# Optimization experiments

Hardware: AMD Instinct MI355X
Metric: run time of the kernel (lower is better)

The kernel has to match this reference:

```python
import jax, jax.numpy as jnp
import numpy as np

NUM_SEGMENTS = 2048
EPS = 1e-6

def setup_inputs() -> dict:
    key = jax.random.key(0)
    k1, k2 = jax.random.split(key)
    N, D = 1000000, 64
    x = jax.random.normal(k1, (N, D), dtype=jnp.float32)
    seg = jnp.sort(jax.random.randint(k2, (N,), 0, NUM_SEGMENTS, dtype=jnp.int32))
    return {"x": x, "seg": seg}

def reference(x, seg):
    # Per-segment SCALAR min/max over all nodes and features of each graph,
    # matching torch's x.min()/x.max() on each unbatched segment.
    row_min = jnp.min(x, axis=1)  # [N]
    row_max = jnp.max(x, axis=1)  # [N]
    g_min = jax.ops.segment_min(row_min, seg, num_segments=NUM_SEGMENTS)  # [G]
    g_max = jax.ops.segment_max(row_max, seg, num_segments=NUM_SEGMENTS)  # [G]
    mn = g_min[seg][:, None]  # [N,1]
    mx = g_max[seg][:, None]  # [N,1]
    return (x - mn) / (mx - mn + EPS)
```

## Files before the change

### kernel.cpp

```cpp
#include <hip/hip_runtime.h>

#define NSEG 2048
#define EPS 1e-6f

__device__ __forceinline__ unsigned enc(float f) {
    unsigned u = __float_as_uint(f);
    return (u & 0x80000000u) ? ~u : (u | 0x80000000u);
}
__device__ __forceinline__ float dec(unsigned k) {
    unsigned u = (k & 0x80000000u) ? (k & 0x7FFFFFFFu) : ~k;
    return __uint_as_float(u);
}

__global__ void init_k(unsigned* __restrict__ mn_k, unsigned* __restrict__ mx_k) {
    int i = blockIdx.x * blockDim.x + threadIdx.x;
    if (i < NSEG) {
        mn_k[i] = 0xFFFFFFFFu;
        mx_k[i] = 0u;
    }
}

__global__ __launch_bounds__(256) void pass1(const float4* __restrict__ x4,
                                             const int* __restrict__ seg,
                                             unsigned* __restrict__ mn_k,
                                             unsigned* __restrict__ mx_k,
                                             int nrows) {
    int row = blockIdx.x * 256 + threadIdx.x;
    if (row >= nrows) return;
    const float4* xr = x4 + (long)row * 16;
    float lmin = INFINITY, lmax = -INFINITY;
#pragma unroll
    for (int j = 0; j < 16; ++j) {
        float4 v = xr[j];
        lmin = fminf(lmin, fminf(fminf(v.x, v.y), fminf(v.z, v.w)));
        lmax = fmaxf(lmax, fmaxf(fmaxf(v.x, v.y), fmaxf(v.z, v.w)));
    }
    int s = seg[row];
    int first = __shfl(s, 0);
    if (__all(s == first)) {
#pragma unroll
        for (int off = 32; off; off >>= 1) {
            lmin = fminf(lmin, __shfl_xor(lmin, off));
            lmax = fmaxf(lmax, __shfl_xor(lmax, off));
        }
        if ((threadIdx.x & 63) == 0) {
            atomicMin(&mn_k[first], enc(lmin));
            atomicMax(&mx_k[first], enc(lmax));
        }
    } else {
        atomicMin(&mn_k[s], enc(lmin));
        atomicMax(&mx_k[s], enc(lmax));
    }
}

__global__ void scalek(const unsigned* __restrict__ mn_k,
                       const unsigned* __restrict__ mx_k,
                       float2* __restrict__ prm) {
    int i = blockIdx.x * blockDim.x + threadIdx.x;
    if (i < NSEG) {
        float mn = dec(mn_k[i]);
        float mx = dec(mx_k[i]);
        float2 p;
        p.x = mn;
        p.y = 1.0f / (mx - mn + EPS);
        prm[i] = p;
    }
}

__global__ __launch_bounds__(256) void pass2(const float4* __restrict__ x4,
                                             const int* __restrict__ seg,
                                             const float2* __restrict__ prm,
                                             float4* __restrict__ out4,
                                             long n4) {
    long g = (long)blockIdx.x * 256 + threadIdx.x;
    if (g >= n4) return;
    int row = (int)(g >> 4);
    int s = seg[row];
    float2 p = prm[s];
    float4 v = x4[g];
    float4 o;
    o.x = (v.x - p.x) * p.y;
    o.y = (v.y - p.x) * p.y;
    o.z = (v.z - p.x) * p.y;
    o.w = (v.w - p.x) * p.y;
    out4[g] = o;
}

extern "C" void kernel_launch(void* const* d_in, const int* in_sizes, int n_in,
                              void* d_out, int out_size, void* d_ws, size_t ws_size,
                              hipStream_t stream) {
    const float* x = (const float*)d_in[0];
    const int* seg = (const int*)d_in[1];
    float* out = (float*)d_out;

    const int nrows = in_sizes[1];
    const long n4 = (long)out_size / 4;

    unsigned* mn_k = (unsigned*)d_ws;
    unsigned* mx_k = mn_k + NSEG;
    float2* prm = (float2*)(mx_k + NSEG);

    init_k<<<(NSEG + 255) / 256, 256, 0, stream>>>(mn_k, mx_k);

    int blocks1 = (nrows + 255) / 256;
    pass1<<<blocks1, 256, 0, stream>>>((const float4*)x, seg, mn_k, mx_k, nrows);

    scalek<<<(NSEG + 255) / 256, 256, 0, stream>>>(mn_k, mx_k, prm);

    long blocks2 = (n4 + 255) / 256;
    pass2<<<(int)blocks2, 256, 0, stream>>>((const float4*)x, seg, prm,
                                            (float4*)out, n4);
}
```

Measured before the change: 532.2 us.

## Coalesce pass1 row-tile loads with segment-uniform fast path; nontemporal output stores

Pass1 now has each block read its 256-row tile as contiguous float4s striped across threads, replacing the old layout where each thread read one 256-byte row. When the first and last rows of the tile share a segment, it reduces the whole tile and does one atomic pair per wave. Otherwise it runs per-chunk wave checks and accumulates runs of the same segment before issuing atomics. Pass2 writes its output with nontemporal stores so the 256MB result does not evict the input from cache.

```diff
diff --git a/kernel.cpp b/kernel.cpp
--- a/kernel.cpp
+++ b/kernel.cpp
@@ -2,6 +2,10 @@
 
 #define NSEG 2048
 #define EPS 1e-6f
+#define TROWS 256
+#define TF4 (TROWS * 16)
+
+typedef float nfloat4 __attribute__((ext_vector_type(4)));
 
 __device__ __forceinline__ unsigned enc(float f) {
     unsigned u = __float_as_uint(f);
@@ -20,36 +24,85 @@
     }
 }
 
+__device__ __forceinline__ void wave_reduce(float& mn, float& mx) {
+#pragma unroll
+    for (int off = 32; off; off >>= 1) {
+        mn = fminf(mn, __shfl_xor(mn, off));
+        mx = fmaxf(mx, __shfl_xor(mx, off));
+    }
+}
+
 __global__ __launch_bounds__(256) void pass1(const float4* __restrict__ x4,
                                              const int* __restrict__ seg,
                                              unsigned* __restrict__ mn_k,
                                              unsigned* __restrict__ mx_k,
                                              int nrows) {
-    int row = blockIdx.x * 256 + threadIdx.x;
-    if (row >= nrows) return;
-    const float4* xr = x4 + (long)row * 16;
-    float lmin = INFINITY, lmax = -INFINITY;
+    const long n4 = (long)nrows * 16;
+    const long base = (long)blockIdx.x * TF4;
+    const int t = threadIdx.x;
+    const int row0 = blockIdx.x * TROWS;
+    const int rlast = min(row0 + TROWS, nrows) - 1;
+    const int sf = seg[row0];
+    const int sl = seg[rlast];
+
+    if (sf == sl) {
+        float lmin = INFINITY, lmax = -INFINITY;
 #pragma unroll
-    for (int j = 0; j < 16; ++j) {
-        float4 v = xr[j];
-        lmin = fminf(lmin, fminf(fminf(v.x, v.y), fminf(v.z, v.w)));
-        lmax = fmaxf(lmax, fmaxf(fmaxf(v.x, v.y), fmaxf(v.z, v.w)));
-    }
-    int s = seg[row];
-    int first = __shfl(s, 0);
-    if (__all(s == first)) {
-#pragma unroll
-        for (int off = 32; off; off >>= 1) {
-            lmin = fminf(lmin, __shfl_xor(lmin, off));
-            lmax = fmaxf(lmax, __shfl_xor(lmax, off));
+        for (int i = 0; i < 16; ++i) {
+            long f = base + (long)i * 256 + t;
+            if (f < n4) {
+                float4 v = x4[f];
+                lmin = fminf(lmin, fminf(fminf(v.x, v.y), fminf(v.z, v.w)));
+                lmax = fmaxf(lmax, fmaxf(fmaxf(v.x, v.y), fmaxf(v.z, v.w)));
+            }
         }
-        if ((threadIdx.x & 63) == 0) {
-            atomicMin(&mn_k[first], enc(lmin));
-            atomicMax(&mx_k[first], enc(lmax));
+        wave_reduce(lmin, lmax);
+        if ((t & 63) == 0) {
+            atomicMin(&mn_k[sf], enc(lmin));
+            atomicMax(&mx_k[sf], enc(lmax));
         }
     } else {
-        atomicMin(&mn_k[s], enc(lmin));
-        atomicMax(&mx_k[s], enc(lmax));
+        float amin = INFINITY, amax = -INFINITY;
+        int as = -1;
+#pragma unroll
+        for (int i = 0; i < 16; ++i) {
+            long f = base + (long)i * 256 + t;
+            bool valid = f < n4;
+            float lmin = INFINITY, lmax = -INFINITY;
+            int s = -1;
+            if (valid) {
+                float4 v = x4[f];
+                lmin = fminf(fminf(v.x, v.y), fminf(v.z, v.w));
+                lmax = fmaxf(fmaxf(v.x, v.y), fmaxf(v.z, v.w));
+                s = seg[(int)(f >> 4)];
+            }
+            int s0 = __shfl(s, 0);
+            if (__all(s == s0 || !valid)) {
+                if (s0 < 0) continue;
+                wave_reduce(lmin, lmax);
+                if ((t & 63) == 0) {
+                    if (s0 != as) {
+                        if (as >= 0) {
+                            atomicMin(&mn_k[as], enc(amin));
+                            atomicMax(&mx_k[as], enc(amax));
+                        }
+                        as = s0; amin = lmin; amax = lmax;
+                    } else {
+                        amin = fminf(amin, lmin);
+                        amax = fmaxf(amax, lmax);
+                    }
+                }
+            } else {
+                if (valid) {
+                    atomicMin(&mn_k[s], enc(lmin));
+                    atomicMax(&mx_k[s], enc(lmax));
+                }
+            }
+        }
+        if ((t & 63) == 0 && as >= 0) {
+            atomicMin(&mn_k[as], enc(amin));
+            atomicMax(&mx_k[as], enc(amax));
+        }
     }
 }
 
@@ -70,7 +123,7 @@
 __global__ __launch_bounds__(256) void pass2(const float4* __restrict__ x4,
                                              const int* __restrict__ seg,
                                              const float2* __restrict__ prm,
-                                             float4* __restrict__ out4,
+                                             nfloat4* __restrict__ out4,
                                              long n4) {
     long g = (long)blockIdx.x * 256 + threadIdx.x;
     if (g >= n4) return;
@@ -78,12 +131,12 @@
     int s = seg[row];
     float2 p = prm[s];
     float4 v = x4[g];
-    float4 o;
+    nfloat4 o;
     o.x = (v.x - p.x) * p.y;
     o.y = (v.y - p.x) * p.y;
     o.z = (v.z - p.x) * p.y;
     o.w = (v.w - p.x) * p.y;
-    out4[g] = o;
+    __builtin_nontemporal_store(o, &out4[g]);
 }
 
 extern "C" void kernel_launch(void* const* d_in, const int* in_sizes, int n_in,
@@ -102,12 +155,12 @@
 
     init_k<<<(NSEG + 255) / 256, 256, 0, stream>>>(mn_k, mx_k);
 
-    int blocks1 = (nrows + 255) / 256;
+    int blocks1 = (nrows + TROWS - 1) / TROWS;
     pass1<<<blocks1, 256, 0, stream>>>((const float4*)x, seg, mn_k, mx_k, nrows);
 
     scalek<<<(NSEG + 255) / 256, 256, 0, stream>>>(mn_k, mx_k, prm);
 
     long blocks2 = (n4 + 255) / 256;
     pass2<<<(int)blocks2, 256, 0, stream>>>((const float4*)x, seg, prm,
-                                            (float4*)out, n4);
+                                            (nfloat4*)out, n4);
 }
```

Result: faster. 472.4 us (-11.2%).
